# Performance work log

Measured on AMD Instinct MI355X. Metric: run time of the kernel, lower is better.

The kernel has to match this reference:

```python
import jax, jax.numpy as jnp
import numpy as np

TEMPERATURE = 0.1
NUM_GROUPS = 1024  # must match fill_max of `groups`


def setup_inputs() -> dict:
    key = jax.random.key(0)
    k1, k2, k3 = jax.random.split(key, 3)
    B, N, D = 16, 16384, 128
    embeddings = jax.random.normal(k1, (B, N, D), dtype=jnp.float32)
    groups = jax.random.randint(k2, (B, N), 0, NUM_GROUPS, dtype=jnp.int32)
    mask = jax.random.randint(k3, (B, N), 0, 2, dtype=jnp.int32).astype(bool)
    return {"embeddings": embeddings, "groups": groups, "mask": mask}


def reference(embeddings, groups, mask):
    # Vectorized equivalent of the per-group python loop:
    # sort nodes by group, positives = roll-by-1 within each group block,
    # negatives = uniform sample from the complement of the anchor's group.
    B, N, D = embeddings.shape
    G = NUM_GROUPS
    emb = embeddings.reshape(B * N, D)
    g = groups.reshape(B * N)
    m = mask.reshape(B * N)
    total = B * N

    # masked-out nodes get sentinel group G -> sorted to the tail, excluded everywhere
    g_eff = jnp.where(m, g, G).astype(jnp.int32)
    order = jnp.argsort(g_eff)            # stable sort by group
    sg = g_eff[order]                     # sorted group labels
    counts = jax.ops.segment_sum(jnp.ones(total, jnp.int32), g_eff,
                                 num_segments=G + 1)
    starts = jnp.searchsorted(sg, jnp.arange(G + 1, dtype=jnp.int32))
    valid_total = total - counts[G]       # number of unmasked nodes

    gi = sg                               # group of element at each sorted position
    cnt = counts[gi]
    st = starts[gi]
    local = jnp.arange(total, dtype=jnp.int32) - st
    # positive partner: previous element in group, wrapping (torch.roll shifts=1)
    partner_local = jnp.mod(local - 1, jnp.maximum(cnt, 1))
    pos_idx = order[st + partner_local]
    anchor_idx = order

    # negative: uniform index into complement (all unmasked nodes not in group gi)
    comp = jnp.maximum(valid_total - cnt, 1)
    u = jax.random.uniform(jax.random.key(42), (total,))
    r = jnp.minimum((u * comp.astype(jnp.float32)).astype(jnp.int32), comp - 1)
    neg_pos = jnp.where(r < st, r, r + cnt)          # skip this group's block
    neg_idx = order[jnp.clip(neg_pos, 0, total - 1)]

    valid = (gi < G) & (cnt >= 2) & ((valid_total - cnt) > 0)

    a = emb[anchor_idx]
    p = emb[pos_idx]
    n = emb[neg_idx]
    pos_score = jnp.sum(a * p, axis=1) / TEMPERATURE
    neg_score = jnp.sum(a * n, axis=1) / TEMPERATURE
    # CE with label 0 over logits [pos, neg]: -log_softmax(...)[0]
    loss_i = jnp.logaddexp(pos_score, neg_score) - pos_score
    vw = valid.astype(loss_i.dtype)
    loss = jnp.sum(loss_i * vw) / jnp.maximum(jnp.sum(vw), 1.0)
    return loss
```

## Files before the change

### kernel.cpp

```cpp
#include <hip/hip_runtime.h>
#include <stdint.h>

#define TOTAL  262144
#define HALF   131072
#define G      1024
#define NBINS  1025
#define NCHUNK 512
#define CHUNK  512

#define OFF_COUNTS 0
#define OFF_STARTS 8192
#define OFF_VT     16388
#define OFF_LOSS   16392
#define OFF_VALID  16400
#define OFF_TICKET 16408
#define OFF_ORDER  16448
#define OFF_GHIST  1065024
#define OFF_BF16   4194304

__device__ __forceinline__ void threefry2x32(uint32_t k0, uint32_t k1,
                                             uint32_t& x0, uint32_t& x1) {
  uint32_t ks0 = k0, ks1 = k1, ks2 = k0 ^ k1 ^ 0x1BD11BDAu;
#define TF_RND(R) { x0 += x1; x1 = (x1 << (R)) | (x1 >> (32 - (R))); x1 ^= x0; }
  x0 += ks0; x1 += ks1;
  TF_RND(13) TF_RND(15) TF_RND(26) TF_RND(6)
  x0 += ks1; x1 += ks2 + 1u;
  TF_RND(17) TF_RND(29) TF_RND(16) TF_RND(24)
  x0 += ks2; x1 += ks0 + 2u;
  TF_RND(13) TF_RND(15) TF_RND(26) TF_RND(6)
  x0 += ks0; x1 += ks1 + 3u;
  TF_RND(17) TF_RND(29) TF_RND(16) TF_RND(24)
  x0 += ks1; x1 += ks2 + 4u;
  TF_RND(13) TF_RND(15) TF_RND(26) TF_RND(6)
  x0 += ks2; x1 += ks0 + 5u;
#undef TF_RND
}

__device__ __forceinline__ int load_mask(const void* mask, int is8, int j) {
  return is8 ? (int)((const unsigned char*)mask)[j] : ((const int*)mask)[j];
}

__device__ __forceinline__ int detect_is8(const void* mask) {
  int lane = threadIdx.x & 63;
  uchar4 p = ((const uchar4*)mask)[lane];
  unsigned long long bal = __ballot((p.y | p.z | p.w) != 0);
  return bal != 0ull;
}

__device__ __forceinline__ uint32_t bf16rne(float f) {
  uint32_t u = __float_as_uint(f);
  return (u + 0x7FFFu + ((u >> 16) & 1u)) >> 16;
}
__device__ __forceinline__ uint32_t pack2(float lo, float hi) {
  return bf16rne(lo) | (bf16rne(hi) << 16);
}
__device__ __forceinline__ float dotu(uint32_t a, uint32_t b) {
  float alo = __uint_as_float(a << 16), ahi = __uint_as_float(a & 0xFFFF0000u);
  float blo = __uint_as_float(b << 16), bhi = __uint_as_float(b & 0xFFFF0000u);
  return alo * blo + ahi * bhi;
}
__device__ __forceinline__ float dot8(uint4 a, uint4 b) {
  return dotu(a.x, b.x) + dotu(a.y, b.y) + dotu(a.z, b.z) + dotu(a.w, b.w);
}

__global__ __launch_bounds__(512) void k_convhist(const float4* __restrict__ e4,
                                                  const int* __restrict__ groups,
                                                  const void* __restrict__ mask,
                                                  int* __restrict__ counts,
                                                  int* __restrict__ ghist,
                                                  uint4* __restrict__ bt) {
  __shared__ int h[NBINS];
  int t = threadIdx.x;
  int c = blockIdx.x;
  int is8 = detect_is8(mask);
  for (int b = t; b < NBINS; b += 512) h[b] = 0;
  __syncthreads();
  int j = c * CHUNK + t;
  int m = load_mask(mask, is8, j);
  int g = m ? groups[j] : G;
  atomicAdd(&h[g], 1);
  size_t base = (size_t)c * 16384;
#pragma unroll 4
  for (int k = 0; k < 16; k++) {
    size_t i4 = base + (size_t)k * 1024 + 2 * t;
    float4 f0 = e4[i4], f1 = e4[i4 + 1];
    uint4 o;
    o.x = pack2(f0.x, f0.y); o.y = pack2(f0.z, f0.w);
    o.z = pack2(f1.x, f1.y); o.w = pack2(f1.z, f1.w);
    bt[base / 2 + (size_t)k * 512 + t] = o;
  }
  __syncthreads();
  for (int b = t; b < NBINS; b += 512) {
    int v = h[b];
    ghist[b * NCHUNK + c] = v;
    if (v) atomicAdd(&counts[b], v);
  }
}

__global__ __launch_bounds__(256) void k_rebase(const int* __restrict__ counts,
                                                int* __restrict__ starts,
                                                int* __restrict__ vtp,
                                                int* __restrict__ ghist) {
  __shared__ int stl[NBINS];
  int t = threadIdx.x;
  int wave = t >> 6, lane = t & 63;
  if (wave == 0) {
    int cr[16];
    int s = 0;
#pragma unroll
    for (int k = 0; k < 16; k++) { cr[k] = counts[lane * 16 + k]; s += cr[k]; }
    int incl = s;
    for (int d = 1; d < 64; d <<= 1) {
      int tt = __shfl_up(incl, d);
      if (lane >= d) incl += tt;
    }
    int run = incl - s;
#pragma unroll
    for (int k = 0; k < 16; k++) {
      stl[lane * 16 + k] = run;
      if (blockIdx.x == 0) starts[lane * 16 + k] = run;
      run += cr[k];
    }
    if (lane == 63) {
      stl[1024] = run;
      if (blockIdx.x == 0) { starts[1024] = run; *vtp = run; }
    }
  }
  __syncthreads();
  int g = blockIdx.x * 4 + wave;
  if (g < NBINS) {
    int* row = ghist + g * NCHUNK;
    int v[8];
    int s = 0;
    int bi = lane * 8;
#pragma unroll
    for (int k = 0; k < 8; k++) { v[k] = row[bi + k]; s += v[k]; }
    int incl = s;
    for (int d = 1; d < 64; d <<= 1) {
      int tt = __shfl_up(incl, d);
      if (lane >= d) incl += tt;
    }
    int run = stl[g] + (incl - s);
#pragma unroll
    for (int k = 0; k < 8; k++) { int tt = v[k]; row[bi + k] = run; run += tt; }
  }
}

__global__ __launch_bounds__(CHUNK) void k_scatter(const int* __restrict__ groups,
                                                   const void* __restrict__ mask,
                                                   const int* __restrict__ ghist,
                                                   int* __restrict__ order) {
  __shared__ int h[8][NBINS];
  int t = threadIdx.x;
  int wave = t >> 6, lane = t & 63;
  int is8 = detect_is8(mask);
  int j = blockIdx.x * CHUNK + t;
  int m = load_mask(mask, is8, j);
  int g = m ? groups[j] : G;
  for (int idx = t; idx < 8 * NBINS; idx += CHUNK) ((int*)h)[idx] = 0;
  __syncthreads();
  unsigned long long mm = ~0ull;
#pragma unroll
  for (int b = 0; b < 11; b++) {
    unsigned long long bal = __ballot(((g >> b) & 1) != 0);
    mm &= ((g >> b) & 1) ? bal : ~bal;
  }
  unsigned long long lt = (1ull << lane) - 1ull;
  int lanerank = __popcll(mm & lt);
  if (lanerank == 0) h[wave][g] = __popcll(mm);
  __syncthreads();
  int rank = lanerank;
  for (int w = 0; w < wave; w++) rank += h[w][g];
  int pos = ghist[g * NCHUNK + blockIdx.x] + rank;
  order[pos] = j;
}

__global__ __launch_bounds__(256) void k_main(const uint4* __restrict__ bt,
                                              const int* __restrict__ groups,
                                              const void* __restrict__ mask,
                                              const int* __restrict__ counts,
                                              const int* __restrict__ starts,
                                              const int* __restrict__ vtp,
                                              const int* __restrict__ order,
                                              double* __restrict__ lossAcc,
                                              double* __restrict__ validAcc,
                                              unsigned int* __restrict__ ticket,
                                              float* __restrict__ out) {
  __shared__ int mA[128], mP[128], mN[128], mF[128];
  __shared__ float bl[4], bv[4];
  int t = threadIdx.x;
  int wave = t >> 6, lane = t & 63;
  int vt = *vtp;
  int P0 = blockIdx.x * 128;

  if (P0 < vt) {
    int is8 = detect_is8(mask);
    if (lane < 32) {
      int i = P0 + wave * 32 + lane;
      int slot = wave * 32 + lane;
      if (i < vt) {
        int j = order[i];
        int mm2 = load_mask(mask, is8, j);
        int g = mm2 ? groups[j] : G;
        int cnt = counts[g], st = starts[g];
        int local = i - st;
        int partner_pos = (local == 0) ? (st + cnt - 1) : (i - 1);
        int pos_idx = order[partner_pos];

        uint32_t x0, x1;
        if (i < HALF) { x0 = (uint32_t)i; x1 = (uint32_t)(i + HALF); }
        else          { x0 = (uint32_t)(i - HALF); x1 = (uint32_t)i; }
        threefry2x32(0u, 42u, x0, x1);
        uint32_t bits = (i < HALF) ? x0 : x1;
        float u = __uint_as_float((bits >> 9) | 0x3F800000u) - 1.0f;

        int compi = vt - cnt;
        int comp = compi > 1 ? compi : 1;
        int r = (int)(u * (float)comp);
        int cm1 = comp - 1;
        if (r > cm1) r = cm1;
        int neg_pos = (r < st) ? r : (r + cnt);
        if (neg_pos < 0) neg_pos = 0;
        if (neg_pos > TOTAL - 1) neg_pos = TOTAL - 1;
        int neg_idx = order[neg_pos];
        int valid = (g < G) && (cnt >= 2) && (compi > 0);
        int shufok = (partner_pos == i - 1);

        mA[slot] = j; mP[slot] = pos_idx; mN[slot] = neg_idx;
        mF[slot] = valid | (shufok << 1);
      } else {
        mA[slot] = 0; mP[slot] = 0; mN[slot] = 0; mF[slot] = 0;
      }
    }
    __syncthreads();

    int sg = lane >> 3, sl = lane & 7;
    float lsum = 0.f, vsum = 0.f;
#pragma unroll 1
    for (int it = 0; it < 4; it++) {
      int slot = wave * 32 + it * 8 + sg;
      int ai = mA[slot], pi = mP[slot], ni = mN[slot], fl = mF[slot];
      int ab = ai * 16 + sl * 2;
      int nb = ni * 16 + sl * 2;
      uint4 a0 = bt[ab], a1 = bt[ab + 1];
      uint4 n0 = bt[nb], n1 = bt[nb + 1];
      uint4 p0, p1;
      p0.x = __shfl_up(a0.x, 8); p0.y = __shfl_up(a0.y, 8);
      p0.z = __shfl_up(a0.z, 8); p0.w = __shfl_up(a0.w, 8);
      p1.x = __shfl_up(a1.x, 8); p1.y = __shfl_up(a1.y, 8);
      p1.z = __shfl_up(a1.z, 8); p1.w = __shfl_up(a1.w, 8);
      if (!((sg > 0) && (fl & 2))) {
        int pb = pi * 16 + sl * 2;
        p0 = bt[pb]; p1 = bt[pb + 1];
      }
      float ap = dot8(a0, p0) + dot8(a1, p1);
      float an = dot8(a0, n0) + dot8(a1, n1);
      ap += __shfl_xor(ap, 4); an += __shfl_xor(an, 4);
      ap += __shfl_xor(ap, 2); an += __shfl_xor(an, 2);
      ap += __shfl_xor(ap, 1); an += __shfl_xor(an, 1);
      if ((fl & 1) && sl == 0) {
        float ps = ap * 10.0f, ns = an * 10.0f;
        float dd = ns - ps;
        float li = fmaxf(dd, 0.0f) + log1pf(expf(-fabsf(dd)));
        lsum += li; vsum += 1.0f;
      }
    }
    for (int d = 32; d >= 1; d >>= 1) {
      lsum += __shfl_xor(lsum, d);
      vsum += __shfl_xor(vsum, d);
    }
    if (lane == 0) { bl[wave] = lsum; bv[wave] = vsum; }
    __syncthreads();
    if (t == 0) {
      float L = bl[0] + bl[1] + bl[2] + bl[3];
      float V = bv[0] + bv[1] + bv[2] + bv[3];
      atomicAdd(lossAcc, (double)L);
      atomicAdd(validAcc, (double)V);
    }
  }

  if (t == 0) {
    __threadfence();
    unsigned int old = atomicAdd(ticket, 1u);
    if (old == gridDim.x - 1) {
      double L = atomicAdd(lossAcc, 0.0);
      double V = atomicAdd(validAcc, 0.0);
      if (V < 1.0) V = 1.0;
      out[0] = (float)(L / V);
    }
  }
}

extern "C" void kernel_launch(void* const* d_in, const int* in_sizes, int n_in,
                              void* d_out, int out_size, void* d_ws, size_t ws_size,
                              hipStream_t stream) {
  const float* emb = (const float*)d_in[0];
  const int* groups = (const int*)d_in[1];
  const void* mask = d_in[2];
  float* out = (float*)d_out;

  char* ws = (char*)d_ws;
  int* counts = (int*)(ws + OFF_COUNTS);
  int* starts = (int*)(ws + OFF_STARTS);
  int* vt = (int*)(ws + OFF_VT);
  double* lossAcc = (double*)(ws + OFF_LOSS);
  double* validAcc = (double*)(ws + OFF_VALID);
  unsigned int* ticket = (unsigned int*)(ws + OFF_TICKET);
  int* order = (int*)(ws + OFF_ORDER);
  int* ghist = (int*)(ws + OFF_GHIST);
  uint4* bt = (uint4*)(ws + OFF_BF16);

  hipMemsetAsync(ws, 0, 16416, stream);

  k_convhist<<<NCHUNK, 512, 0, stream>>>((const float4*)emb, groups, mask,
                                         counts, ghist, bt);
  k_rebase<<<(NBINS + 3) / 4, 256, 0, stream>>>(counts, starts, vt, ghist);
  k_scatter<<<NCHUNK, CHUNK, 0, stream>>>(groups, mask, ghist, order);
  k_main<<<TOTAL / 128, 256, 0, stream>>>(bt, groups, mask, counts, starts,
                                          vt, order, lossAcc, validAcc,
                                          ticket, out);
}
```

Measured before the change: 293.1 us.

## Skip masked-row conversion, prefetch bf16 table into cache, widen per-lane row loads

The conversion kernel now writes bf16 rows only for unmasked nodes, cutting write and read traffic for rows that are never gathered. The scatter kernel then streams the whole bf16 table into a dummy accumulator so it is resident in L2/MALL before the gather kernel runs. The main kernel handles two rows per 4-lane group with all loads issued up front, raising memory-level parallelism. The prefetch adds a full extra read pass, and the skipped rows leave stale data in the workspace.

```diff
diff --git a/kernel.cpp b/kernel.cpp
--- a/kernel.cpp
+++ b/kernel.cpp
@@ -14,6 +14,7 @@
 #define OFF_LOSS   16392
 #define OFF_VALID  16400
 #define OFF_TICKET 16408
+#define OFF_SINK   16416
 #define OFF_ORDER  16448
 #define OFF_GHIST  1065024
 #define OFF_BF16   4194304
@@ -70,6 +71,7 @@
                                                   int* __restrict__ ghist,
                                                   uint4* __restrict__ bt) {
   __shared__ int h[NBINS];
+  __shared__ unsigned char sm[CHUNK];
   int t = threadIdx.x;
   int c = blockIdx.x;
   int is8 = detect_is8(mask);
@@ -78,18 +80,22 @@
   int j = c * CHUNK + t;
   int m = load_mask(mask, is8, j);
   int g = m ? groups[j] : G;
+  sm[t] = (unsigned char)(m != 0);
   atomicAdd(&h[g], 1);
+  __syncthreads();
   size_t base = (size_t)c * 16384;
 #pragma unroll 4
   for (int k = 0; k < 16; k++) {
-    size_t i4 = base + (size_t)k * 1024 + 2 * t;
-    float4 f0 = e4[i4], f1 = e4[i4 + 1];
-    uint4 o;
-    o.x = pack2(f0.x, f0.y); o.y = pack2(f0.z, f0.w);
-    o.z = pack2(f1.x, f1.y); o.w = pack2(f1.z, f1.w);
-    bt[base / 2 + (size_t)k * 512 + t] = o;
-  }
-  __syncthreads();
+    int row_local = k * 32 + (t >> 4);
+    if (sm[row_local]) {
+      size_t i4 = base + (size_t)k * 1024 + 2 * t;
+      float4 f0 = e4[i4], f1 = e4[i4 + 1];
+      uint4 o;
+      o.x = pack2(f0.x, f0.y); o.y = pack2(f0.z, f0.w);
+      o.z = pack2(f1.x, f1.y); o.w = pack2(f1.z, f1.w);
+      bt[base / 2 + (size_t)k * 512 + t] = o;
+    }
+  }
   for (int b = t; b < NBINS; b += 512) {
     int v = h[b];
     ghist[b * NCHUNK + c] = v;
@@ -149,7 +155,9 @@
 __global__ __launch_bounds__(CHUNK) void k_scatter(const int* __restrict__ groups,
                                                    const void* __restrict__ mask,
                                                    const int* __restrict__ ghist,
-                                                   int* __restrict__ order) {
+                                                   int* __restrict__ order,
+                                                   const uint4* __restrict__ bt,
+                                                   float* __restrict__ sink) {
   __shared__ int h[8][NBINS];
   int t = threadIdx.x;
   int wave = t >> 6, lane = t & 63;
@@ -173,6 +181,15 @@
   for (int w = 0; w < wave; w++) rank += h[w][g];
   int pos = ghist[g * NCHUNK + blockIdx.x] + rank;
   order[pos] = j;
+
+  size_t n4 = (size_t)TOTAL * 16;
+  float acc = 0.f;
+  for (size_t idx = (size_t)blockIdx.x * CHUNK + t; idx < n4;
+       idx += (size_t)gridDim.x * CHUNK) {
+    uint4 v = bt[idx];
+    acc += (float)(v.x ^ v.y ^ v.z ^ v.w);
+  }
+  if (acc == 1.2345678e18f) sink[0] = acc;
 }
 
 __global__ __launch_bounds__(256) void k_main(const uint4* __restrict__ bt,
@@ -234,35 +251,70 @@
     }
     __syncthreads();
 
-    int sg = lane >> 3, sl = lane & 7;
+    int sg = lane >> 2, sl = lane & 3;
+    int slot0 = wave * 32 + (sg << 1);
+    int slot1 = slot0 + 1;
+    int a0i = mA[slot0], n0i = mN[slot0], f0 = mF[slot0];
+    int a1i = mA[slot1], n1i = mN[slot1], f1 = mF[slot1];
+    uint4 A0[4], A1[4], N0[4], N1[4];
+    {
+      int ab0 = a0i * 16 + sl * 4;
+      int ab1 = a1i * 16 + sl * 4;
+      int nb0 = n0i * 16 + sl * 4;
+      int nb1 = n1i * 16 + sl * 4;
+#pragma unroll
+      for (int k = 0; k < 4; k++) {
+        A0[k] = bt[ab0 + k];
+        A1[k] = bt[ab1 + k];
+        N0[k] = bt[nb0 + k];
+        N1[k] = bt[nb1 + k];
+      }
+    }
+    uint4 Pv0[4], Pv1[4];
+#pragma unroll
+    for (int k = 0; k < 4; k++) {
+      Pv0[k].x = __shfl_up(A1[k].x, 4);
+      Pv0[k].y = __shfl_up(A1[k].y, 4);
+      Pv0[k].z = __shfl_up(A1[k].z, 4);
+      Pv0[k].w = __shfl_up(A1[k].w, 4);
+    }
+    if (!((sg > 0) && (f0 & 2))) {
+      int pb = mP[slot0] * 16 + sl * 4;
+#pragma unroll
+      for (int k = 0; k < 4; k++) Pv0[k] = bt[pb + k];
+    }
+    if (f1 & 2) {
+#pragma unroll
+      for (int k = 0; k < 4; k++) Pv1[k] = A0[k];
+    } else {
+      int pb = mP[slot1] * 16 + sl * 4;
+#pragma unroll
+      for (int k = 0; k < 4; k++) Pv1[k] = bt[pb + k];
+    }
+    float ap0 = 0.f, an0 = 0.f, ap1 = 0.f, an1 = 0.f;
+#pragma unroll
+    for (int k = 0; k < 4; k++) {
+      ap0 += dot8(A0[k], Pv0[k]);
+      an0 += dot8(A0[k], N0[k]);
+      ap1 += dot8(A1[k], Pv1[k]);
+      an1 += dot8(A1[k], N1[k]);
+    }
+    ap0 += __shfl_xor(ap0, 2); an0 += __shfl_xor(an0, 2);
+    ap1 += __shfl_xor(ap1, 2); an1 += __shfl_xor(an1, 2);
+    ap0 += __shfl_xor(ap0, 1); an0 += __shfl_xor(an0, 1);
+    ap1 += __shfl_xor(ap1, 1); an1 += __shfl_xor(an1, 1);
+
     float lsum = 0.f, vsum = 0.f;
-#pragma unroll 1
-    for (int it = 0; it < 4; it++) {
-      int slot = wave * 32 + it * 8 + sg;
-      int ai = mA[slot], pi = mP[slot], ni = mN[slot], fl = mF[slot];
-      int ab = ai * 16 + sl * 2;
-      int nb = ni * 16 + sl * 2;
-      uint4 a0 = bt[ab], a1 = bt[ab + 1];
-      uint4 n0 = bt[nb], n1 = bt[nb + 1];
-      uint4 p0, p1;
-      p0.x = __shfl_up(a0.x, 8); p0.y = __shfl_up(a0.y, 8);
-      p0.z = __shfl_up(a0.z, 8); p0.w = __shfl_up(a0.w, 8);
-      p1.x = __shfl_up(a1.x, 8); p1.y = __shfl_up(a1.y, 8);
-      p1.z = __shfl_up(a1.z, 8); p1.w = __shfl_up(a1.w, 8);
-      if (!((sg > 0) && (fl & 2))) {
-        int pb = pi * 16 + sl * 2;
-        p0 = bt[pb]; p1 = bt[pb + 1];
+    if (sl == 0) {
+      if (f0 & 1) {
+        float dd = (an0 - ap0) * 10.0f;
+        lsum += fmaxf(dd, 0.0f) + log1pf(expf(-fabsf(dd)));
+        vsum += 1.0f;
       }
-      float ap = dot8(a0, p0) + dot8(a1, p1);
-      float an = dot8(a0, n0) + dot8(a1, n1);
-      ap += __shfl_xor(ap, 4); an += __shfl_xor(an, 4);
-      ap += __shfl_xor(ap, 2); an += __shfl_xor(an, 2);
-      ap += __shfl_xor(ap, 1); an += __shfl_xor(an, 1);
-      if ((fl & 1) && sl == 0) {
-        float ps = ap * 10.0f, ns = an * 10.0f;
-        float dd = ns - ps;
-        float li = fmaxf(dd, 0.0f) + log1pf(expf(-fabsf(dd)));
-        lsum += li; vsum += 1.0f;
+      if (f1 & 1) {
+        float dd = (an1 - ap1) * 10.0f;
+        lsum += fmaxf(dd, 0.0f) + log1pf(expf(-fabsf(dd)));
+        vsum += 1.0f;
       }
     }
     for (int d = 32; d >= 1; d >>= 1) {
@@ -306,16 +358,17 @@
   double* lossAcc = (double*)(ws + OFF_LOSS);
   double* validAcc = (double*)(ws + OFF_VALID);
   unsigned int* ticket = (unsigned int*)(ws + OFF_TICKET);
+  float* sink = (float*)(ws + OFF_SINK);
   int* order = (int*)(ws + OFF_ORDER);
   int* ghist = (int*)(ws + OFF_GHIST);
   uint4* bt = (uint4*)(ws + OFF_BF16);
 
-  hipMemsetAsync(ws, 0, 16416, stream);
+  hipMemsetAsync(ws, 0, 16432, stream);
 
   k_convhist<<<NCHUNK, 512, 0, stream>>>((const float4*)emb, groups, mask,
                                          counts, ghist, bt);
   k_rebase<<<(NBINS + 3) / 4, 256, 0, stream>>>(counts, starts, vt, ghist);
-  k_scatter<<<NCHUNK, CHUNK, 0, stream>>>(groups, mask, ghist, order);
+  k_scatter<<<NCHUNK, CHUNK, 0, stream>>>(groups, mask, ghist, order, bt, sink);
   k_main<<<TOTAL / 128, 256, 0, stream>>>(bt, groups, mask, counts, starts,
                                           vt, order, lossAcc, validAcc,
                                           ticket, out);
```

Result: no change. 289.7 us (-1.2%).
